# Kernel optimization log

Measured on AMD Instinct MI355X. Metric: run time of the kernel, lower is better.

## Reference

```python
import jax, jax.numpy as jnp
import numpy as np

T = 1_048_576          # sequence length
NUM_INPUTS = 16        # symbol vocab for _delta table
MAX_OUTPUT = 25        # softmax width / counter range


def setup_inputs() -> dict:
    key = jax.random.key(0)
    k1, k2, k3 = jax.random.split(key, 3)
    input_seq = jax.random.randint(k1, (T,), 0, NUM_INPUTS)
    # learned params (random instead of the degenerate zero init so the
    # recurrence and softmax are non-trivial)
    delta = jax.random.normal(k2, (NUM_INPUTS,), dtype=jnp.float32) * 0.5
    out_bias = jax.random.normal(k3, (MAX_OUTPUT,), dtype=jnp.float32) * 0.1
    out_scale = jnp.ones((1,), dtype=jnp.float32)
    return {"input_seq": input_seq, "delta": delta,
            "out_bias": out_bias, "out_scale": out_scale}


def reference(input_seq, delta, out_bias, out_scale):
    max_out = out_bias.shape[0]
    # per-step increments: vectorized gather  [T]
    deltas = delta[input_seq]

    # scalar counter recurrence with clamp (non-associative -> lax.scan)
    def step(c, d):
        c = jnp.clip(c + d, 0.0, float(max_out - 1))
        return c, c

    _, counters = jax.lax.scan(step, jnp.float32(0.0), deltas)  # [T]

    # vectorized readout: distances [T, max_out] -> logits -> softmax
    positions = jnp.arange(max_out, dtype=jnp.float32)
    distances = jnp.abs(positions[None, :] - counters[:, None])
    logits = -distances * out_scale + out_bias
    return jax.nn.softmax(logits, axis=-1)  # [T, max_out]
```

## Files before the change

### kernel.cpp

```cpp
#include <hip/hip_runtime.h>

#define T_LEN   1048576
#define SEG     256
#define NSEG    (T_LEN / SEG)
#define MAXO    25
#define CLAMP_HI 24.0f
#define BIGF    1e30f

struct Trip { float a, l, h; };

__device__ __forceinline__ Trip comb(Trip x, Trip y) {
    Trip r;
    r.a = x.a + y.a;
    r.l = fmaxf(x.l + y.a, y.l);
    r.h = fminf(fmaxf(x.h + y.a, y.l), y.h);
    return r;
}
__device__ __forceinline__ float applyT(Trip p, float c) {
    return fminf(fmaxf(c + p.a, p.l), p.h);
}
__device__ __forceinline__ Trip shflUpTrip(Trip v, int off) {
    Trip r;
    r.a = __shfl_up(v.a, off, 64);
    r.l = __shfl_up(v.l, off, 64);
    r.h = __shfl_up(v.h, off, 64);
    return r;
}

__global__ __launch_bounds__(256)
void k1_seg(const int* __restrict__ seq, const float* __restrict__ delta,
            float* __restrict__ tri) {
    __shared__ float dl[16];
    const int tid = threadIdx.x, lane = tid & 63;
    if (tid < 16) dl[tid] = delta[tid];
    __syncthreads();

    const int4 s4 = *(const int4*)(seq + blockIdx.x * 1024 + tid * 4);
    Trip t = {dl[s4.x], 0.0f, CLAMP_HI};
    { Trip e = {dl[s4.y], 0.0f, CLAMP_HI}; t = comb(t, e); }
    { Trip e = {dl[s4.z], 0.0f, CLAMP_HI}; t = comb(t, e); }
    { Trip e = {dl[s4.w], 0.0f, CLAMP_HI}; t = comb(t, e); }

#pragma unroll
    for (int off = 1; off < 64; off <<= 1) {
        Trip o = shflUpTrip(t, off);
        if (lane >= off) t = comb(o, t);
    }
    if (lane == 63) {
        const int sid = blockIdx.x * 4 + (tid >> 6);
        tri[3 * sid + 0] = t.a;
        tri[3 * sid + 1] = t.l;
        tri[3 * sid + 2] = t.h;
    }
}

__global__ __launch_bounds__(1024)
void k2_scan(const float* __restrict__ tri, float* __restrict__ entry) {
    __shared__ Trip agg[16];
    const int tid = threadIdx.x, lane = tid & 63, wid = tid >> 6;

    const float4* p = (const float4*)(tri + tid * 12);
    const float4 f0 = p[0], f1 = p[1], f2 = p[2];
    const Trip t0 = {f0.x, f0.y, f0.z};
    const Trip t1 = {f0.w, f1.x, f1.y};
    const Trip t2 = {f1.z, f1.w, f2.x};
    const Trip t3 = {f2.y, f2.z, f2.w};

    Trip incl = comb(comb(comb(t0, t1), t2), t3);
#pragma unroll
    for (int off = 1; off < 64; off <<= 1) {
        Trip o = shflUpTrip(incl, off);
        if (lane >= off) incl = comb(o, incl);
    }
    if (lane == 63) agg[wid] = incl;
    __syncthreads();

    Trip W = {0.0f, -BIGF, BIGF};
    for (int w = 0; w < wid; ++w) W = comb(W, agg[w]);
    const Trip prev = shflUpTrip(incl, 1);
    const Trip E = (lane == 0) ? W : comb(W, prev);

    float c = applyT(E, 0.0f);
    entry[4 * tid + 0] = c;
    c = applyT(t0, c); entry[4 * tid + 1] = c;
    c = applyT(t1, c); entry[4 * tid + 2] = c;
    c = applyT(t2, c); entry[4 * tid + 3] = c;
}

__global__ __launch_bounds__(256)
void k3_out(const int* __restrict__ seq, const float* __restrict__ delta,
            const float* __restrict__ bias, const float* __restrict__ scale,
            const float* __restrict__ entry, float* __restrict__ out) {
    __shared__ float tile[SEG * MAXO];
    __shared__ Trip agg[4];
    __shared__ float dl[16], bs[MAXO];

    const int tid = threadIdx.x, lane = tid & 63, wid = tid >> 6;
    const int bid = blockIdx.x;

    if (tid < 16)   dl[tid] = delta[tid];
    if (tid < MAXO) bs[tid] = bias[tid];
    const float sfac = scale[0];
    const float cseg = entry[bid];
    const int s = seq[bid * SEG + tid];
    __syncthreads();

    Trip t = {dl[s], 0.0f, CLAMP_HI};
#pragma unroll
    for (int off = 1; off < 64; off <<= 1) {
        Trip o = shflUpTrip(t, off);
        if (lane >= off) t = comb(o, t);
    }
    if (lane == 63) agg[wid] = t;
    __syncthreads();

    float cb = cseg;
    for (int w = 0; w < wid; ++w) cb = applyT(agg[w], cb);
    const float c = applyT(t, cb);

    float ev[MAXO];
    float sum = 0.0f;
#pragma unroll
    for (int j = 0; j < MAXO; ++j) {
        ev[j] = __expf(fmaf(-sfac, fabsf((float)j - c), bs[j]));
        sum += ev[j];
    }
    const float r = 1.0f / sum;
#pragma unroll
    for (int j = 0; j < MAXO; ++j)
        tile[tid * MAXO + j] = ev[j] * r;
    __syncthreads();

    const float4* tp = (const float4*)tile;
    float4* op = (float4*)(out + (size_t)bid * SEG * MAXO);
#pragma unroll
    for (int i = tid; i < SEG * MAXO / 4; i += 256)
        op[i] = tp[i];
}

extern "C" void kernel_launch(void* const* d_in, const int* in_sizes, int n_in,
                              void* d_out, int out_size, void* d_ws, size_t ws_size,
                              hipStream_t stream) {
    const int*   seq   = (const int*)d_in[0];
    const float* delta = (const float*)d_in[1];
    const float* bias  = (const float*)d_in[2];
    const float* scale = (const float*)d_in[3];
    float* out = (float*)d_out;

    float* tri   = (float*)d_ws;
    float* entry = tri + NSEG * 3;

    k1_seg <<<T_LEN / 1024, 256, 0, stream>>>(seq, delta, tri);
    k2_scan<<<1, 1024, 0, stream>>>(tri, entry);
    k3_out <<<NSEG, 256, 0, stream>>>(seq, delta, bias, scale, entry, out);
}
```

Before: 123.5 us.

## Fuse three-pass scan into single-pass decoupled look-back kernel

Replaces the segment-reduce, single-block scan, and output kernels with one kernel that uses a ticket-ordered decoupled look-back scan over clamp-triple aggregates. Each block handles 1024 rows, computes entry counters locally, and writes softmax output through a wave-local shared tile with no extra block barrier per row chunk. This removes two kernel launches, the serial single-block scan, and the reread of the input sequence. In exchange it adds a memset, atomic flag spinning, and a serial 64-step combine in the look-back loop, and each block now processes four times as many rows.

```diff
diff --git a/kernel.cpp b/kernel.cpp
--- a/kernel.cpp
+++ b/kernel.cpp
@@ -1,11 +1,15 @@
 #include <hip/hip_runtime.h>
 
-#define T_LEN   1048576
-#define SEG     256
-#define NSEG    (T_LEN / SEG)
-#define MAXO    25
-#define CLAMP_HI 24.0f
-#define BIGF    1e30f
+#define T_LEN      1048576
+#define TILE_ROWS  1024
+#define NTILES     (T_LEN / TILE_ROWS)
+#define MAXO       25
+#define CLAMP_HI   24.0f
+#define BIGF       1e30f
+
+#define FLAG_NONE 0u
+#define FLAG_PART 1u
+#define FLAG_INC  2u
 
 struct Trip { float a, l, h; };
 
@@ -26,116 +30,137 @@
     r.h = __shfl_up(v.h, off, 64);
     return r;
 }
-
-__global__ __launch_bounds__(256)
-void k1_seg(const int* __restrict__ seq, const float* __restrict__ delta,
-            float* __restrict__ tri) {
-    __shared__ float dl[16];
-    const int tid = threadIdx.x, lane = tid & 63;
-    if (tid < 16) dl[tid] = delta[tid];
-    __syncthreads();
-
-    const int4 s4 = *(const int4*)(seq + blockIdx.x * 1024 + tid * 4);
-    Trip t = {dl[s4.x], 0.0f, CLAMP_HI};
-    { Trip e = {dl[s4.y], 0.0f, CLAMP_HI}; t = comb(t, e); }
-    { Trip e = {dl[s4.z], 0.0f, CLAMP_HI}; t = comb(t, e); }
-    { Trip e = {dl[s4.w], 0.0f, CLAMP_HI}; t = comb(t, e); }
-
-#pragma unroll
-    for (int off = 1; off < 64; off <<= 1) {
-        Trip o = shflUpTrip(t, off);
-        if (lane >= off) t = comb(o, t);
-    }
-    if (lane == 63) {
-        const int sid = blockIdx.x * 4 + (tid >> 6);
-        tri[3 * sid + 0] = t.a;
-        tri[3 * sid + 1] = t.l;
-        tri[3 * sid + 2] = t.h;
-    }
-}
-
-__global__ __launch_bounds__(1024)
-void k2_scan(const float* __restrict__ tri, float* __restrict__ entry) {
-    __shared__ Trip agg[16];
-    const int tid = threadIdx.x, lane = tid & 63, wid = tid >> 6;
-
-    const float4* p = (const float4*)(tri + tid * 12);
-    const float4 f0 = p[0], f1 = p[1], f2 = p[2];
-    const Trip t0 = {f0.x, f0.y, f0.z};
-    const Trip t1 = {f0.w, f1.x, f1.y};
-    const Trip t2 = {f1.z, f1.w, f2.x};
-    const Trip t3 = {f2.y, f2.z, f2.w};
-
-    Trip incl = comb(comb(comb(t0, t1), t2), t3);
-#pragma unroll
-    for (int off = 1; off < 64; off <<= 1) {
-        Trip o = shflUpTrip(incl, off);
-        if (lane >= off) incl = comb(o, incl);
-    }
-    if (lane == 63) agg[wid] = incl;
-    __syncthreads();
-
-    Trip W = {0.0f, -BIGF, BIGF};
-    for (int w = 0; w < wid; ++w) W = comb(W, agg[w]);
-    const Trip prev = shflUpTrip(incl, 1);
-    const Trip E = (lane == 0) ? W : comb(W, prev);
-
-    float c = applyT(E, 0.0f);
-    entry[4 * tid + 0] = c;
-    c = applyT(t0, c); entry[4 * tid + 1] = c;
-    c = applyT(t1, c); entry[4 * tid + 2] = c;
-    c = applyT(t2, c); entry[4 * tid + 3] = c;
+__device__ __forceinline__ Trip shflTrip(Trip v, int src) {
+    Trip r;
+    r.a = __shfl(v.a, src, 64);
+    r.l = __shfl(v.l, src, 64);
+    r.h = __shfl(v.h, src, 64);
+    return r;
 }
 
 __global__ __launch_bounds__(256)
-void k3_out(const int* __restrict__ seq, const float* __restrict__ delta,
-            const float* __restrict__ bias, const float* __restrict__ scale,
-            const float* __restrict__ entry, float* __restrict__ out) {
-    __shared__ float tile[SEG * MAXO];
-    __shared__ Trip agg[4];
+void k_fused(const int* __restrict__ seq, const float* __restrict__ delta,
+             const float* __restrict__ bias, const float* __restrict__ scale,
+             unsigned* __restrict__ ticket, unsigned* __restrict__ flags,
+             float* __restrict__ partA, float* __restrict__ inclA,
+             float* __restrict__ out)
+{
+    __shared__ float tile[256 * MAXO];
+    __shared__ float c_arr[TILE_ROWS];
+    __shared__ Trip  agg[4];
+    __shared__ Trip  Esh;
     __shared__ float dl[16], bs[MAXO];
+    __shared__ unsigned bidsh;
 
     const int tid = threadIdx.x, lane = tid & 63, wid = tid >> 6;
-    const int bid = blockIdx.x;
 
+    if (tid == 0) bidsh = atomicAdd(ticket, 1u);
     if (tid < 16)   dl[tid] = delta[tid];
     if (tid < MAXO) bs[tid] = bias[tid];
     const float sfac = scale[0];
-    const float cseg = entry[bid];
-    const int s = seq[bid * SEG + tid];
+    __syncthreads();
+    const int bid = (int)bidsh;
+
+    const int4 s4 = *(const int4*)(seq + bid * TILE_ROWS + tid * 4);
+    const Trip t0 = {dl[s4.x], 0.0f, CLAMP_HI};
+    const Trip t1 = {dl[s4.y], 0.0f, CLAMP_HI};
+    const Trip t2 = {dl[s4.z], 0.0f, CLAMP_HI};
+    const Trip t3 = {dl[s4.w], 0.0f, CLAMP_HI};
+
+    Trip inc = comb(comb(t0, t1), comb(t2, t3));
+#pragma unroll
+    for (int off = 1; off < 64; off <<= 1) {
+        Trip o = shflUpTrip(inc, off);
+        if (lane >= off) inc = comb(o, inc);
+    }
+    if (lane == 63) agg[wid] = inc;
     __syncthreads();
 
-    Trip t = {dl[s], 0.0f, CLAMP_HI};
-#pragma unroll
-    for (int off = 1; off < 64; off <<= 1) {
-        Trip o = shflUpTrip(t, off);
-        if (lane >= off) t = comb(o, t);
+    const Trip P = comb(comb(agg[0], agg[1]), comb(agg[2], agg[3]));
+
+    if (wid == 0) {
+        if (lane == 0) {
+            partA[3*bid+0] = P.a; partA[3*bid+1] = P.l; partA[3*bid+2] = P.h;
+            __hip_atomic_store(&flags[bid], FLAG_PART, __ATOMIC_RELEASE,
+                               __HIP_MEMORY_SCOPE_AGENT);
+        }
+        Trip E = {0.0f, -BIGF, BIGF};
+        int look = bid - 1;
+        while (look >= 0) {
+            const int pred = look - lane;
+            unsigned f = FLAG_INC;
+            Trip tp = {0.0f, -BIGF, BIGF};
+            if (pred >= 0) {
+                int guard = 0;
+                for (;;) {
+                    f = __hip_atomic_load(&flags[pred], __ATOMIC_ACQUIRE,
+                                          __HIP_MEMORY_SCOPE_AGENT);
+                    if (f != FLAG_NONE || ++guard >= (1 << 20)) break;
+                }
+                const float* src = (f == FLAG_INC) ? (inclA + 3*pred)
+                                                   : (partA + 3*pred);
+                tp.a = src[0]; tp.l = src[1]; tp.h = src[2];
+            }
+            const unsigned long long m = __ballot(f == FLAG_INC);
+            if (m) {
+                const int d = __ffsll(m) - 1;
+                Trip acc = shflTrip(tp, d);
+                for (int i = d - 1; i >= 0; --i) acc = comb(acc, shflTrip(tp, i));
+                E = comb(acc, E);
+                break;
+            } else {
+                Trip acc = shflTrip(tp, 63);
+                for (int i = 62; i >= 0; --i) acc = comb(acc, shflTrip(tp, i));
+                E = comb(acc, E);
+                look -= 64;
+            }
+        }
+        if (lane == 0) {
+            const Trip I = comb(E, P);
+            inclA[3*bid+0] = I.a; inclA[3*bid+1] = I.l; inclA[3*bid+2] = I.h;
+            __hip_atomic_store(&flags[bid], FLAG_INC, __ATOMIC_RELEASE,
+                               __HIP_MEMORY_SCOPE_AGENT);
+            Esh = E;
+        }
     }
-    if (lane == 63) agg[wid] = t;
     __syncthreads();
 
-    float cb = cseg;
+    float cb = applyT(Esh, 0.0f);
     for (int w = 0; w < wid; ++w) cb = applyT(agg[w], cb);
-    const float c = applyT(t, cb);
-
-    float ev[MAXO];
-    float sum = 0.0f;
-#pragma unroll
-    for (int j = 0; j < MAXO; ++j) {
-        ev[j] = __expf(fmaf(-sfac, fabsf((float)j - c), bs[j]));
-        sum += ev[j];
-    }
-    const float r = 1.0f / sum;
-#pragma unroll
-    for (int j = 0; j < MAXO; ++j)
-        tile[tid * MAXO + j] = ev[j] * r;
+    const Trip prev = shflUpTrip(inc, 1);
+    const float c_in = (lane == 0) ? cb : applyT(prev, cb);
+    float4 cv;
+    cv.x = applyT(t0, c_in);
+    cv.y = applyT(t1, cv.x);
+    cv.z = applyT(t2, cv.y);
+    cv.w = applyT(t3, cv.z);
+    *(float4*)(c_arr + 4 * tid) = cv;
     __syncthreads();
 
-    const float4* tp = (const float4*)tile;
-    float4* op = (float4*)(out + (size_t)bid * SEG * MAXO);
+    const size_t outbase = (size_t)bid * TILE_ROWS * MAXO;
+#pragma unroll 1
+    for (int r = 0; r < 4; ++r) {
+        const float c = c_arr[r * 256 + tid];
+        float ev[MAXO];
+        float sum = 0.0f;
 #pragma unroll
-    for (int i = tid; i < SEG * MAXO / 4; i += 256)
-        op[i] = tp[i];
+        for (int j = 0; j < MAXO; ++j) {
+            ev[j] = __expf(fmaf(-sfac, fabsf((float)j - c), bs[j]));
+            sum += ev[j];
+        }
+        const float rinv = 1.0f / sum;
+#pragma unroll
+        for (int j = 0; j < MAXO; ++j)
+            tile[tid * MAXO + j] = ev[j] * rinv;
+
+        const float4* tp4 = (const float4*)(tile + wid * 64 * MAXO);
+        float4* op4 = (float4*)(out + outbase + (size_t)(r * 256 + wid * 64) * MAXO);
+#pragma unroll
+        for (int k = 0; k < 7; ++k) {
+            const int idx = lane + k * 64;
+            if (idx < 400) op4[idx] = tp4[idx];
+        }
+    }
 }
 
 extern "C" void kernel_launch(void* const* d_in, const int* in_sizes, int n_in,
@@ -147,10 +172,12 @@
     const float* scale = (const float*)d_in[3];
     float* out = (float*)d_out;
 
-    float* tri   = (float*)d_ws;
-    float* entry = tri + NSEG * 3;
+    unsigned* ticket = (unsigned*)d_ws;
+    unsigned* flags  = (unsigned*)((char*)d_ws + 256);
+    float*    partA  = (float*)((char*)d_ws + 4608);
+    float*    inclA  = partA + 3 * NTILES;
 
-    k1_seg <<<T_LEN / 1024, 256, 0, stream>>>(seq, delta, tri);
-    k2_scan<<<1, 1024, 0, stream>>>(tri, entry);
-    k3_out <<<NSEG, 256, 0, stream>>>(seq, delta, bias, scale, entry, out);
+    hipMemsetAsync(d_ws, 0, 4608, stream);
+    k_fused<<<NTILES, 256, 0, stream>>>(seq, delta, bias, scale,
+                                        ticket, flags, partA, inclA, out);
 }
```

After: 218.8 us. +77.1%, slower.
